# Kernel tuning notes

Hardware: AMD Instinct MI355X
Metric: run time of the kernel (lower is better)

## Reference

```python
import jax, jax.numpy as jnp
import numpy as np

N_GRAPHS = 1000
P = 300                 # nodes per ring graph
N = N_GRAPHS * P        # 300000 nodes
IN_DIM = 2
HID = 128
OUT_DIM = 2


def _ring_edges():
    idx = jnp.arange(N)
    g = idx // P
    pos = idx % P
    nxt = g * P + (pos + 1) % P
    src = jnp.concatenate([idx, nxt])
    dst = jnp.concatenate([nxt, idx])
    return jnp.stack([src, dst]), g


def setup_inputs() -> dict:
    key = jax.random.key(0)
    ks = jax.random.split(key, 11)
    edge_index, batch = _ring_edges()
    x = jax.random.normal(ks[0], (N, IN_DIM), jnp.float32)

    def glorot(k, fan_in, fan_out):
        lim = np.sqrt(6.0 / (fan_in + fan_out)).astype(np.float32)
        return jax.random.uniform(k, (fan_in, fan_out), jnp.float32, -lim, lim)

    return {
        "x": x,
        "edge_index": edge_index,
        "batch": batch,
        "W1": glorot(ks[1], IN_DIM, HID), "b1": jnp.zeros((HID,), jnp.float32),
        "W2": glorot(ks[2], HID, HID),    "b2": jnp.zeros((HID,), jnp.float32),
        "W3": glorot(ks[3], HID, HID),    "b3": jnp.zeros((HID,), jnp.float32),
        "fw1": glorot(ks[4], HID, HID),   "fb1": jnp.zeros((HID,), jnp.float32),
        "fw2": glorot(ks[5], HID, OUT_DIM), "fb2": jnp.zeros((OUT_DIM,), jnp.float32),
    }


def _gcn_conv(x, W, b, src, dst, norm):
    h = x @ W                              # [N, out]
    msg = h[src] * norm[:, None]           # gather + per-edge scale
    agg = jax.ops.segment_sum(msg, dst, num_segments=N)  # scatter-add
    return agg + b


def reference(x, edge_index, batch, W1, b1, W2, b2, W3, b3, fw1, fb1, fw2, fb2):
    loop = jnp.arange(N)
    src = jnp.concatenate([edge_index[0], loop])
    dst = jnp.concatenate([edge_index[1], loop])
    deg = jax.ops.segment_sum(jnp.ones_like(dst, jnp.float32), dst, num_segments=N)
    dis = jax.lax.rsqrt(deg)               # deg >= 1 due to self-loops
    norm = dis[src] * dis[dst]             # per-edge normalization

    h = jax.nn.relu(_gcn_conv(x, W1, b1, src, dst, norm))
    h = jax.nn.relu(_gcn_conv(h, W2, b2, src, dst, norm))
    h = jax.nn.relu(_gcn_conv(h, W3, b3, src, dst, norm))

    # global mean pool per graph
    sums = jax.ops.segment_sum(h, batch, num_segments=N_GRAPHS)
    cnts = jax.ops.segment_sum(jnp.ones((N,), jnp.float32), batch, num_segments=N_GRAPHS)
    pooled = sums / cnts[:, None]

    out = jax.nn.relu(pooled @ fw1 + fb1)
    out = out @ fw2 + fb2
    return out
```

## Files before the change

kernel.cpp:

```cpp
#include <hip/hip_runtime.h>
#include <stdint.h>

#define P    300
#define HID  128
#define NG   1000
#define NTL  19

typedef __attribute__((ext_vector_type(8))) short bf16x8;
typedef __attribute__((ext_vector_type(4))) float f32x4;

__device__ short g_wsw[2 * HID * HID];

__device__ __forceinline__ short f2bf(float f) {
    union { float f; uint32_t u; } v; v.f = f;
    uint32_t r = v.u + 0x7fffu + ((v.u >> 16) & 1u);
    return (short)(r >> 16);
}

__global__ __launch_bounds__(256) void k_prep(const float* __restrict__ W2,
                                              const float* __restrict__ W3) {
    int b = blockIdx.x;
    const float* W = (b < 8) ? W2 : W3;
    short* dst = g_wsw + ((b < 8) ? 0 : HID * HID);
    int t  = (b & 7) * 256 + threadIdx.x;
    int f  = t >> 4;
    int kc = t & 15;
    bf16x8 o;
    #pragma unroll
    for (int j = 0; j < 8; ++j)
        o[j] = f2bf(W[(kc * 8 + j) * HID + f]);
    *(bf16x8*)&dst[(f * 16 + (kc ^ (f & 15))) * 8] = o;
}

__device__ __forceinline__ void avg_epi(const float* G, float vp0, float vn3,
                                        float b, float* o) {
    o[0] = (vp0  + G[0] + G[1]) * (1.0f / 3.0f) + b;
    o[1] = (G[0] + G[1] + G[2]) * (1.0f / 3.0f) + b;
    o[2] = (G[1] + G[2] + G[3]) * (1.0f / 3.0f) + b;
    o[3] = (G[2] + G[3] + vn3 ) * (1.0f / 3.0f) + b;
    #pragma unroll
    for (int i = 0; i < 4; ++i) o[i] = o[i] > 0.f ? o[i] : 0.f;
}

__device__ __forceinline__ void store4(short* __restrict__ buf, int nt16,
                                       int q, int lm, int ftg, const float* o) {
    int fh = ftg * 2 + (lm >> 3), fl = lm & 7;
    #pragma unroll
    for (int i = 0; i < 4; ++i) {
        int node = nt16 + q * 4 + i;
        buf[(node * 16 + (fh ^ (node & 15))) * 8 + fl] = f2bf(o[i]);
    }
}

template<int POOL>
__device__ __forceinline__ void run_pass(short* __restrict__ buf,
                                         const short* __restrict__ wbase,
                                         const float* __restrict__ bias,
                                         float* __restrict__ pool, int tid) {
    const int lane = tid & 63, u = tid >> 6, q = lane >> 4, lm = lane & 15;
    const int ftg0 = u * 2;
    bf16x8 wf[2][4];
    #pragma unroll
    for (int ft = 0; ft < 2; ++ft) {
        int f = (ftg0 + ft) * 16 + lm;
        #pragma unroll
        for (int kk = 0; kk < 4; ++kk)
            wf[ft][kk] = *(const bf16x8*)&wbase[(f * 16 + ((4 * kk + q) ^ lm)) * 8];
    }
    float biaf[2] = { bias[ftg0 * 16 + lm], bias[ftg0 * 16 + 16 + lm] };
    const int sA = (q == 0) ? (48 + lm) : (lane - 16);
    const int sB = (lane + 16) & 63;

    f32x4 Gp[2], Gc[2], Gfirst[2];
    float c15[2] = {0.f, 0.f}, r0G1[2] = {0.f, 0.f};
    float psum[2] = {0.f, 0.f};

    Gp[0] = f32x4{0.f,0.f,0.f,0.f}; Gp[1] = f32x4{0.f,0.f,0.f,0.f};
    #pragma unroll
    for (int kk = 0; kk < 4; ++kk) {
        bf16x8 af = *(const bf16x8*)&buf[(lm * 16 + ((4 * kk + q) ^ lm)) * 8];
        Gp[0] = __builtin_amdgcn_mfma_f32_16x16x32_bf16(af, wf[0][kk], Gp[0], 0, 0, 0);
        Gp[1] = __builtin_amdgcn_mfma_f32_16x16x32_bf16(af, wf[1][kk], Gp[1], 0, 0, 0);
    }
    Gfirst[0] = Gp[0]; Gfirst[1] = Gp[1];

    for (int t = 1; t < NTL; ++t) {
        if (!POOL) __syncthreads();
        const short* tb = buf + t * 2048;
        Gc[0] = f32x4{0.f,0.f,0.f,0.f}; Gc[1] = f32x4{0.f,0.f,0.f,0.f};
        #pragma unroll
        for (int kk = 0; kk < 4; ++kk) {
            bf16x8 af = *(const bf16x8*)&tb[(lm * 16 + ((4 * kk + q) ^ lm)) * 8];
            Gc[0] = __builtin_amdgcn_mfma_f32_16x16x32_bf16(af, wf[0][kk], Gc[0], 0, 0, 0);
            Gc[1] = __builtin_amdgcn_mfma_f32_16x16x32_bf16(af, wf[1][kk], Gc[1], 0, 0, 0);
        }
        #pragma unroll
        for (int ft = 0; ft < 2; ++ft) {
            float bpA = __shfl(Gp[ft][3], sA, 64);
            float bpB = __shfl(Gp[ft][0], sB, 64);
            float bpC = __shfl(Gc[ft][0], lm, 64);
            if (t == 1) {
                r0G1[ft] = bpC;
            } else {
                float vp0 = (q == 0) ? c15[ft] : bpA;
                float vn3 = (q == 3) ? bpC : bpB;
                float o[4];
                avg_epi((const float*)&Gp[ft], vp0, vn3, biaf[ft], o);
                if (!POOL) store4(buf, (t - 1) * 16, q, lm, ftg0 + ft, o);
                else psum[ft] += o[0] + o[1] + o[2] + o[3];
            }
            c15[ft] = bpA;
        }
        Gp[0] = Gc[0]; Gp[1] = Gc[1];
    }

    if (!POOL) __syncthreads();
    #pragma unroll
    for (int ft = 0; ft < 2; ++ft) {
        float bpA  = __shfl(Gp[ft][3], sA, 64);
        float bpB  = __shfl(Gp[ft][0], sB, 64);
        float g0r0 = __shfl(Gfirst[ft][0], lm, 64);
        float vp0  = (q == 0) ? c15[ft] : bpA;
        float vn3  = (q == 2) ? g0r0 : bpB;
        float o[4];
        avg_epi((const float*)&Gp[ft], vp0, vn3, biaf[ft], o);
        if (q < 3) {
            if (!POOL) store4(buf, 18 * 16, q, lm, ftg0 + ft, o);
            else psum[ft] += o[0] + o[1] + o[2] + o[3];
        }
        float bpW  = __shfl(Gp[ft][3], 32 + lm, 64);
        float bpA0 = __shfl(Gfirst[ft][3], sA, 64);
        float bpB0 = __shfl(Gfirst[ft][0], sB, 64);
        float vp00 = (q == 0) ? bpW : bpA0;
        float vn30 = (q == 3) ? r0G1[ft] : bpB0;
        float o0[4];
        avg_epi((const float*)&Gfirst[ft], vp00, vn30, biaf[ft], o0);
        if (!POOL) store4(buf, 0, q, lm, ftg0 + ft, o0);
        else psum[ft] += o0[0] + o0[1] + o0[2] + o0[3];
    }

    if (POOL) {
        #pragma unroll
        for (int ft = 0; ft < 2; ++ft) {
            psum[ft] += __shfl_xor(psum[ft], 16, 64);
            psum[ft] += __shfl_xor(psum[ft], 32, 64);
        }
        if (q == 0) {
            pool[ftg0 * 16 + lm]      = psum[0];
            pool[ftg0 * 16 + 16 + lm] = psum[1];
        }
    }
}

__global__ __launch_bounds__(256, 2) void k_graph(
        const float* __restrict__ x,
        const float* __restrict__ W1,  const float* __restrict__ b1,
        const float* __restrict__ b2v, const float* __restrict__ b3v,
        const float* __restrict__ fw1, const float* __restrict__ fb1,
        const float* __restrict__ fw2, const float* __restrict__ fb2,
        float* __restrict__ out) {
    __shared__ __align__(16) short buf[304 * HID];
    __shared__ __align__(16) float scr[640];
    float* xs    = scr;
    float* pool  = scr;
    float* parts = scr + 128;
    float* s1    = scr + 384;

    const int g = blockIdx.x, tid = threadIdx.x;

    if (tid < 150) *(float4*)&xs[tid * 4] = *(const float4*)&x[g * 600 + tid * 4];
    __syncthreads();

    {
        const int kc1 = tid & 15;
        const int n0  = tid >> 4;
        float w1x[8], w1y[8], b1v[8];
        #pragma unroll
        for (int j = 0; j < 8; ++j) {
            w1x[j] = W1[kc1 * 8 + j];
            w1y[j] = W1[HID + kc1 * 8 + j];
            b1v[j] = b1[kc1 * 8 + j];
        }
        #pragma unroll
        for (int it = 0; it < NTL; ++it) {
            int node = it * 16 + n0;
            bf16x8 o;
            if (node < P) {
                int prev = (node == 0)     ? P - 1 : node - 1;
                int next = (node == P - 1) ? 0     : node + 1;
                float ax = (xs[2*prev]   + xs[2*node]   + xs[2*next])   * (1.f/3.f);
                float ay = (xs[2*prev+1] + xs[2*node+1] + xs[2*next+1]) * (1.f/3.f);
                #pragma unroll
                for (int j = 0; j < 8; ++j) {
                    float v = ax * w1x[j] + ay * w1y[j] + b1v[j];
                    o[j] = f2bf(v > 0.f ? v : 0.f);
                }
            } else {
                o = bf16x8{0, 0, 0, 0, 0, 0, 0, 0};
            }
            *(bf16x8*)&buf[(node * 16 + (kc1 ^ (node & 15))) * 8] = o;
        }
    }
    __syncthreads();

    run_pass<0>(buf, g_wsw,             b2v, pool, tid);
    __syncthreads();
    run_pass<1>(buf, g_wsw + HID * HID, b3v, pool, tid);
    __syncthreads();

    {
        int f = tid & 127, half = tid >> 7;
        float p = 0.f;
        const float* fw1c = fw1 + f;
        #pragma unroll 4
        for (int k = half * 64; k < half * 64 + 64; ++k)
            p += pool[k] * fw1c[k * 128];
        parts[half * 128 + f] = p;
    }
    __syncthreads();
    if (tid < 128) {
        float o1 = fb1[tid] + (parts[tid] + parts[128 + tid]) * (1.0f / 300.0f);
        s1[tid] = o1 > 0.f ? o1 : 0.f;
    }
    __syncthreads();
    if (tid < 128) {
        int o = tid >> 6, ln = tid & 63;
        float v = s1[ln] * fw2[ln * 2 + o] + s1[ln + 64] * fw2[(ln + 64) * 2 + o];
        #pragma unroll
        for (int off = 1; off <= 32; off <<= 1)
            v += __shfl_xor(v, off, 64);
        if (ln == 0) out[g * 2 + o] = v + fb2[o];
    }
}

extern "C" void kernel_launch(void* const* d_in, const int* in_sizes, int n_in,
                              void* d_out, int out_size, void* d_ws, size_t ws_size,
                              hipStream_t stream) {
    const float* x   = (const float*)d_in[0];
    const float* W1  = (const float*)d_in[3];
    const float* b1  = (const float*)d_in[4];
    const float* W2  = (const float*)d_in[5];
    const float* b2  = (const float*)d_in[6];
    const float* W3  = (const float*)d_in[7];
    const float* b3  = (const float*)d_in[8];
    const float* fw1 = (const float*)d_in[9];
    const float* fb1 = (const float*)d_in[10];
    const float* fw2 = (const float*)d_in[11];
    const float* fb2 = (const float*)d_in[12];
    float* out = (float*)d_out;

    k_prep <<<dim3(16), dim3(256), 0, stream>>>(W2, W3);
    k_graph<<<dim3(NG), dim3(256), 0, stream>>>(x, W1, b1, b2, b3,
                                                fw1, fb1, fw2, fb2, out);
}
```

Measured before the change: 130.3 us.

## Batch two tiles per barrier, pack bf16 feature pairs for shuffles and stores

The GCN pass now computes two node tiles of MFMA results before each barrier. This halves the number of __syncthreads in the in-place LDS pass. W2 columns are permuted at prep time so each lane owns an adjacent feature pair. That lets the epilogue write packed 32-bit bf16 pairs and exchange neighbour values with one shuffle per pair instead of one per feature. The first layer also uses the hardware bf16x2 conversion and a single 128-bit store per node. In exchange, neighbour values passed through shuffles are rounded to bf16 before averaging, which slightly reduces precision.

```diff
diff --git a/kernel.cpp b/kernel.cpp
--- a/kernel.cpp
+++ b/kernel.cpp
@@ -1,4 +1,5 @@
 #include <hip/hip_runtime.h>
+#include <hip/hip_bf16.h>
 #include <stdint.h>
 
 #define P    300
@@ -16,20 +17,38 @@
     uint32_t r = v.u + 0x7fffu + ((v.u >> 16) & 1u);
     return (short)(r >> 16);
 }
+__device__ __forceinline__ float bf2f(short s) {
+    union { uint32_t u; float f; } v; v.u = ((uint32_t)(uint16_t)s) << 16;
+    return v.f;
+}
+__device__ __forceinline__ uint32_t pkbf2(float a, float b) {
+    union { __hip_bfloat162 h; uint32_t u; } cv;
+    cv.h = __float22bfloat162_rn(float2{a, b});
+    return cv.u;
+}
+__device__ __forceinline__ float unpk(int v, int ft) {
+    return bf2f((short)(ft ? (((uint32_t)v) >> 16) : (v & 0xffff)));
+}
 
 __global__ __launch_bounds__(256) void k_prep(const float* __restrict__ W2,
                                               const float* __restrict__ W3) {
     int b = blockIdx.x;
-    const float* W = (b < 8) ? W2 : W3;
-    short* dst = g_wsw + ((b < 8) ? 0 : HID * HID);
-    int t  = (b & 7) * 256 + threadIdx.x;
-    int f  = t >> 4;
-    int kc = t & 15;
+    const bool perm = (b < 8);
+    const float* W = perm ? W2 : W3;
+    short* dst = g_wsw + (perm ? 0 : HID * HID);
+    int t    = (b & 7) * 256 + threadIdx.x;
+    int fkey = t >> 4;
+    int kc   = t & 15;
+    int fsrc;
+    if (perm) {
+        int u = fkey >> 5, ft = (fkey >> 4) & 1, l = fkey & 15;
+        fsrc = u * 32 + 2 * l + ft;
+    } else fsrc = fkey;
     bf16x8 o;
     #pragma unroll
     for (int j = 0; j < 8; ++j)
-        o[j] = f2bf(W[(kc * 8 + j) * HID + f]);
-    *(bf16x8*)&dst[(f * 16 + (kc ^ (f & 15))) * 8] = o;
+        o[j] = f2bf(W[(kc * 8 + j) * HID + fsrc]);
+    *(bf16x8*)&dst[(fkey * 16 + (kc ^ (fkey & 15))) * 8] = o;
 }
 
 __device__ __forceinline__ void avg_epi(const float* G, float vp0, float vn3,
@@ -42,79 +61,87 @@
     for (int i = 0; i < 4; ++i) o[i] = o[i] > 0.f ? o[i] : 0.f;
 }
 
-__device__ __forceinline__ void store4(short* __restrict__ buf, int nt16,
-                                       int q, int lm, int ftg, const float* o) {
-    int fh = ftg * 2 + (lm >> 3), fl = lm & 7;
-    #pragma unroll
-    for (int i = 0; i < 4; ++i) {
-        int node = nt16 + q * 4 + i;
-        buf[(node * 16 + (fh ^ (node & 15))) * 8 + fl] = f2bf(o[i]);
-    }
-}
-
 template<int POOL>
 __device__ __forceinline__ void run_pass(short* __restrict__ buf,
                                          const short* __restrict__ wbase,
                                          const float* __restrict__ bias,
                                          float* __restrict__ pool, int tid) {
-    const int lane = tid & 63, u = tid >> 6, q = lane >> 4, lm = lane & 15;
-    const int ftg0 = u * 2;
+    const int lane = tid & 63, wv = tid >> 6, q = lane >> 4, lm = lane & 15;
+    const int ftg0 = wv * 2;
     bf16x8 wf[2][4];
     #pragma unroll
     for (int ft = 0; ft < 2; ++ft) {
-        int f = (ftg0 + ft) * 16 + lm;
+        int fkey = (ftg0 + ft) * 16 + lm;
         #pragma unroll
         for (int kk = 0; kk < 4; ++kk)
-            wf[ft][kk] = *(const bf16x8*)&wbase[(f * 16 + ((4 * kk + q) ^ lm)) * 8];
-    }
-    float biaf[2] = { bias[ftg0 * 16 + lm], bias[ftg0 * 16 + 16 + lm] };
+            wf[ft][kk] = *(const bf16x8*)&wbase[(fkey * 16 + ((4 * kk + q) ^ lm)) * 8];
+    }
+    float biaf[2];
+    #pragma unroll
+    for (int ft = 0; ft < 2; ++ft)
+        biaf[ft] = POOL ? bias[(ftg0 + ft) * 16 + lm] : bias[wv * 32 + 2 * lm + ft];
     const int sA = (q == 0) ? (48 + lm) : (lane - 16);
     const int sB = (lane + 16) & 63;
-
-    f32x4 Gp[2], Gc[2], Gfirst[2];
+    const int fpair = wv * 32 + 2 * lm;
+    const int kcs = fpair >> 3, offs = fpair & 7;
+
+    f32x4 Gp[2], Ga[2], Gb[2], Gfirst[2];
     float c15[2] = {0.f, 0.f}, r0G1[2] = {0.f, 0.f};
     float psum[2] = {0.f, 0.f};
 
-    Gp[0] = f32x4{0.f,0.f,0.f,0.f}; Gp[1] = f32x4{0.f,0.f,0.f,0.f};
-    #pragma unroll
-    for (int kk = 0; kk < 4; ++kk) {
-        bf16x8 af = *(const bf16x8*)&buf[(lm * 16 + ((4 * kk + q) ^ lm)) * 8];
-        Gp[0] = __builtin_amdgcn_mfma_f32_16x16x32_bf16(af, wf[0][kk], Gp[0], 0, 0, 0);
-        Gp[1] = __builtin_amdgcn_mfma_f32_16x16x32_bf16(af, wf[1][kk], Gp[1], 0, 0, 0);
-    }
-    Gfirst[0] = Gp[0]; Gfirst[1] = Gp[1];
-
-    for (int t = 1; t < NTL; ++t) {
-        if (!POOL) __syncthreads();
+    auto mfma_tile = [&](int t, f32x4* G) {
         const short* tb = buf + t * 2048;
-        Gc[0] = f32x4{0.f,0.f,0.f,0.f}; Gc[1] = f32x4{0.f,0.f,0.f,0.f};
+        G[0] = f32x4{0.f, 0.f, 0.f, 0.f};
+        G[1] = f32x4{0.f, 0.f, 0.f, 0.f};
         #pragma unroll
         for (int kk = 0; kk < 4; ++kk) {
             bf16x8 af = *(const bf16x8*)&tb[(lm * 16 + ((4 * kk + q) ^ lm)) * 8];
-            Gc[0] = __builtin_amdgcn_mfma_f32_16x16x32_bf16(af, wf[0][kk], Gc[0], 0, 0, 0);
-            Gc[1] = __builtin_amdgcn_mfma_f32_16x16x32_bf16(af, wf[1][kk], Gc[1], 0, 0, 0);
-        }
+            G[0] = __builtin_amdgcn_mfma_f32_16x16x32_bf16(af, wf[0][kk], G[0], 0, 0, 0);
+            G[1] = __builtin_amdgcn_mfma_f32_16x16x32_bf16(af, wf[1][kk], G[1], 0, 0, 0);
+        }
+    };
+    auto epi = [&](const f32x4* E, const f32x4* N, int T, bool act) -> int {
+        uint32_t uA = pkbf2(E[0][3], E[1][3]);
+        uint32_t uB = pkbf2(E[0][0], E[1][0]);
+        uint32_t uC = pkbf2(N[0][0], N[1][0]);
+        int vA = __shfl((int)uA, sA, 64);
+        int vB = __shfl((int)uB, sB, 64);
+        int vC = __shfl((int)uC, lm, 64);
+        float o[2][4];
         #pragma unroll
         for (int ft = 0; ft < 2; ++ft) {
-            float bpA = __shfl(Gp[ft][3], sA, 64);
-            float bpB = __shfl(Gp[ft][0], sB, 64);
-            float bpC = __shfl(Gc[ft][0], lm, 64);
-            if (t == 1) {
-                r0G1[ft] = bpC;
-            } else {
-                float vp0 = (q == 0) ? c15[ft] : bpA;
-                float vn3 = (q == 3) ? bpC : bpB;
-                float o[4];
-                avg_epi((const float*)&Gp[ft], vp0, vn3, biaf[ft], o);
-                if (!POOL) store4(buf, (t - 1) * 16, q, lm, ftg0 + ft, o);
-                else psum[ft] += o[0] + o[1] + o[2] + o[3];
+            float bpA = unpk(vA, ft), bpB = unpk(vB, ft), bpC = unpk(vC, ft);
+            float vp0 = (q == 0) ? c15[ft] : bpA;
+            float vn3 = (q == 3) ? bpC : bpB;
+            avg_epi((const float*)&E[ft], vp0, vn3, biaf[ft], o[ft]);
+            c15[ft] = bpA;
+            if (act && POOL) psum[ft] += o[ft][0] + o[ft][1] + o[ft][2] + o[ft][3];
+        }
+        if (act && !POOL) {
+            #pragma unroll
+            for (int i = 0; i < 4; ++i) {
+                int node = T * 16 + q * 4 + i;
+                *(uint32_t*)&buf[(node * 16 + (kcs ^ (node & 15))) * 8 + offs] =
+                    pkbf2(o[0][i], o[1][i]);
             }
-            c15[ft] = bpA;
-        }
-        Gp[0] = Gc[0]; Gp[1] = Gc[1];
-    }
-
-    if (!POOL) __syncthreads();
+        }
+        return vC;
+    };
+
+    mfma_tile(0, Gp);
+    Gfirst[0] = Gp[0]; Gfirst[1] = Gp[1];
+
+    for (int j = 1; j <= 9; ++j) {
+        mfma_tile(2 * j - 1, Ga);
+        mfma_tile(2 * j, Gb);
+        if (!POOL) __syncthreads();
+        int vC0 = epi(Gp, Ga, 2 * j - 2, j > 1);
+        if (j == 1) { r0G1[0] = unpk(vC0, 0); r0G1[1] = unpk(vC0, 1); }
+        epi(Ga, Gb, 2 * j - 1, true);
+        Gp[0] = Gb[0]; Gp[1] = Gb[1];
+    }
+
+    float o18[2][4], o0[2][4];
     #pragma unroll
     for (int ft = 0; ft < 2; ++ft) {
         float bpA  = __shfl(Gp[ft][3], sA, 64);
@@ -122,21 +149,30 @@
         float g0r0 = __shfl(Gfirst[ft][0], lm, 64);
         float vp0  = (q == 0) ? c15[ft] : bpA;
         float vn3  = (q == 2) ? g0r0 : bpB;
-        float o[4];
-        avg_epi((const float*)&Gp[ft], vp0, vn3, biaf[ft], o);
-        if (q < 3) {
-            if (!POOL) store4(buf, 18 * 16, q, lm, ftg0 + ft, o);
-            else psum[ft] += o[0] + o[1] + o[2] + o[3];
-        }
+        avg_epi((const float*)&Gp[ft], vp0, vn3, biaf[ft], o18[ft]);
         float bpW  = __shfl(Gp[ft][3], 32 + lm, 64);
         float bpA0 = __shfl(Gfirst[ft][3], sA, 64);
         float bpB0 = __shfl(Gfirst[ft][0], sB, 64);
         float vp00 = (q == 0) ? bpW : bpA0;
         float vn30 = (q == 3) ? r0G1[ft] : bpB0;
-        float o0[4];
-        avg_epi((const float*)&Gfirst[ft], vp00, vn30, biaf[ft], o0);
-        if (!POOL) store4(buf, 0, q, lm, ftg0 + ft, o0);
-        else psum[ft] += o0[0] + o0[1] + o0[2] + o0[3];
+        avg_epi((const float*)&Gfirst[ft], vp00, vn30, biaf[ft], o0[ft]);
+        if (POOL) {
+            if (q < 3) psum[ft] += o18[ft][0] + o18[ft][1] + o18[ft][2] + o18[ft][3];
+            psum[ft] += o0[ft][0] + o0[ft][1] + o0[ft][2] + o0[ft][3];
+        }
+    }
+    if (!POOL) {
+        #pragma unroll
+        for (int i = 0; i < 4; ++i) {
+            if (q < 3) {
+                int node = 288 + q * 4 + i;
+                *(uint32_t*)&buf[(node * 16 + (kcs ^ (node & 15))) * 8 + offs] =
+                    pkbf2(o18[0][i], o18[1][i]);
+            }
+            int n0 = q * 4 + i;
+            *(uint32_t*)&buf[(n0 * 16 + (kcs ^ (n0 & 15))) * 8 + offs] =
+                pkbf2(o0[0][i], o0[1][i]);
+        }
     }
 
     if (POOL) {
@@ -184,21 +220,26 @@
         #pragma unroll
         for (int it = 0; it < NTL; ++it) {
             int node = it * 16 + n0;
-            bf16x8 o;
+            uint32_t w[4] = {0u, 0u, 0u, 0u};
             if (node < P) {
                 int prev = (node == 0)     ? P - 1 : node - 1;
                 int next = (node == P - 1) ? 0     : node + 1;
-                float ax = (xs[2*prev]   + xs[2*node]   + xs[2*next])   * (1.f/3.f);
-                float ay = (xs[2*prev+1] + xs[2*node+1] + xs[2*next+1]) * (1.f/3.f);
+                float2 xp = *(const float2*)&xs[2 * prev];
+                float2 xc = *(const float2*)&xs[2 * node];
+                float2 xn = *(const float2*)&xs[2 * next];
+                float ax = (xp.x + xc.x + xn.x) * (1.f / 3.f);
+                float ay = (xp.y + xc.y + xn.y) * (1.f / 3.f);
                 #pragma unroll
-                for (int j = 0; j < 8; ++j) {
-                    float v = ax * w1x[j] + ay * w1y[j] + b1v[j];
-                    o[j] = f2bf(v > 0.f ? v : 0.f);
+                for (int jj = 0; jj < 4; ++jj) {
+                    float va = ax * w1x[2*jj]   + ay * w1y[2*jj]   + b1v[2*jj];
+                    float vb = ax * w1x[2*jj+1] + ay * w1y[2*jj+1] + b1v[2*jj+1];
+                    va = va > 0.f ? va : 0.f;
+                    vb = vb > 0.f ? vb : 0.f;
+                    w[jj] = pkbf2(va, vb);
                 }
-            } else {
-                o = bf16x8{0, 0, 0, 0, 0, 0, 0, 0};
             }
-            *(bf16x8*)&buf[(node * 16 + (kc1 ^ (node & 15))) * 8] = o;
+            *(uint4*)&buf[(node * 16 + (kc1 ^ (node & 15))) * 8] =
+                uint4{w[0], w[1], w[2], w[3]};
         }
     }
     __syncthreads();
```

Result: faster. 126.5 us (-2.9%).
